# Kernel tuning notes

Hardware: AMD Instinct MI355X
Metric: run time of the kernel (lower is better)

The kernel has to match this reference:

```python
import jax, jax.numpy as jnp
import numpy as np

B, DIN, D = 1000, 1024, 512
C, L = 1203, 77
N_INS, N_EX = 4, 5
K_SEL, K_TOP = 32, 5
HEADS, DH, MLP, NL = 8, 64, 2048, 4
TEMP = 50.0


def setup_inputs() -> dict:
    key = jax.random.key(0)
    ks = iter(jax.random.split(key, 64))

    def rn(shape, s=0.02):
        return jax.random.normal(next(ks), shape, dtype=jnp.float32) * s

    def layer_params(prefix):
        return {
            prefix + '_ln1_g': jnp.ones((NL, D)), prefix + '_ln1_b': jnp.zeros((NL, D)),
            prefix + '_qkv_w': rn((NL, D, 3 * D)), prefix + '_qkv_b': jnp.zeros((NL, 3 * D)),
            prefix + '_out_w': rn((NL, D, D)), prefix + '_out_b': jnp.zeros((NL, D)),
            prefix + '_ln2_g': jnp.ones((NL, D)), prefix + '_ln2_b': jnp.zeros((NL, D)),
            prefix + '_fc_w': rn((NL, D, MLP)), prefix + '_fc_b': jnp.zeros((NL, MLP)),
            prefix + '_pr_w': rn((NL, MLP, D)), prefix + '_pr_b': jnp.zeros((NL, D)),
        }

    zw = jax.random.normal(next(ks), (D, C + 1), dtype=jnp.float32)
    zw = zw / jnp.linalg.norm(zw, axis=0, keepdims=True)  # F.normalize(dim=0) as in __init__
    inp = {
        'x': jax.random.normal(next(ks), (B, DIN), dtype=jnp.float32),
        'linear_w': rn((DIN, D)), 'linear_b': jnp.zeros((D,)),
        'zs_weight': zw,
        'sample_w': rn((D, D)), 'sample_b': jnp.zeros((D,)),
        'ins_token': rn((N_INS, D), 0.1),
        'token_seq': rn((C, L, D), 0.1),
        'exemplar': rn((C, N_EX, D), 0.1),
        'eos_index': jax.random.randint(next(ks), (C,), 5, 60, dtype=jnp.int32),
    }
    inp.update(layer_params('agg'))
    inp['pos_emb'] = rn((L, D), 0.01)
    inp.update(layer_params('txt'))
    inp['lnf_g'] = jnp.ones((D,))
    inp['lnf_b'] = jnp.zeros((D,))
    inp['text_proj'] = rn((D, D))
    return inp


def layernorm(x, g, b, eps=1e-5):
    m = x.mean(-1, keepdims=True)
    v = x.var(-1, keepdims=True)
    return (x - m) * jax.lax.rsqrt(v + eps) * g + b


def quick_gelu(x):  # CLIP QuickGELU
    return x * jax.nn.sigmoid(1.702 * x)


def transformer(h, ln1g, ln1b, qkvw, qkvb, ow, ob, ln2g, ln2b, fcw, fcb, prw, prb, mask=None):
    # h: [N, S, D]; pre-LN residual attention blocks (CLIP style)
    Bn, S, _ = h.shape
    scale = np.float32(1.0 / np.sqrt(DH))
    for i in range(NL):
        a = layernorm(h, ln1g[i], ln1b[i])
        qkv = a @ qkvw[i] + qkvb[i]
        q, k, v = jnp.split(qkv, 3, axis=-1)
        q = q.reshape(Bn, S, HEADS, DH)
        k = k.reshape(Bn, S, HEADS, DH)
        v = v.reshape(Bn, S, HEADS, DH)
        s = jnp.einsum('bqhd,bkhd->bhqk', q, k) * scale
        if mask is not None:
            s = s + mask
        o = jnp.einsum('bhqk,bkhd->bqhd', jax.nn.softmax(s, axis=-1), v).reshape(Bn, S, D)
        h = h + o @ ow[i] + ob[i]
        m = layernorm(h, ln2g[i], ln2b[i])
        h = h + quick_gelu(m @ fcw[i] + fcb[i]) @ prw[i] + prb[i]
    return h


def inverse_sigmoid(x, eps=1e-5):
    x = jnp.clip(x, 0.0, 1.0)
    x1 = jnp.clip(x, eps, None)
    x2 = jnp.clip(1.0 - x, eps, None)
    return jnp.log(x1 / x2)


def reference(x, linear_w, linear_b, zs_weight, sample_w, sample_b, ins_token, token_seq,
              exemplar, eos_index,
              agg_ln1_g, agg_ln1_b, agg_qkv_w, agg_qkv_b, agg_out_w, agg_out_b,
              agg_ln2_g, agg_ln2_b, agg_fc_w, agg_fc_b, agg_pr_w, agg_pr_b,
              pos_emb, txt_ln1_g, txt_ln1_b, txt_qkv_w, txt_qkv_b, txt_out_w, txt_out_b,
              txt_ln2_g, txt_ln2_b, txt_fc_w, txt_fc_b, txt_pr_w, txt_pr_b,
              lnf_g, lnf_b, text_proj):
    # ---- base classifier ----
    h = x @ linear_w + linear_b                                        # [B, D]
    h = TEMP * h / jnp.linalg.norm(h, axis=1, keepdims=True)
    logits = h @ zs_weight                                             # [B, C+1]
    # ---- entropy-based proposal selection (eval path, k=32) ----
    p = jax.nn.sigmoid(logits)
    entropy = (-p * jax.nn.log_sigmoid(logits)).sum(-1)                # [B]
    _, select_index = jax.lax.top_k(entropy, K_SEL)                    # [32]
    sel_logits = logits[select_index]                                  # [32, C+1]
    _, topk_index = jax.lax.top_k(sel_logits[:, :-1], K_TOP)           # [32, 5]
    sampled_x = jax.lax.stop_gradient(h[select_index]) @ sample_w + sample_b  # [32, D]
    # ---- batched aggregator input (replaces per-proposal python loop) ----
    base = ins_token[None] + (sampled_x / TEMP)[:, None, :]            # [32, N_INS, D]
    base = jnp.broadcast_to(base[:, None], (K_SEL, K_TOP, N_INS, D))
    ex = exemplar[topk_index]                                          # [32, 5, N_EX, D]
    agg_in = jnp.concatenate([base, ex], axis=2).reshape(K_SEL * K_TOP, N_INS + N_EX, D)
    agg_out = transformer(agg_in, agg_ln1_g, agg_ln1_b, agg_qkv_w, agg_qkv_b, agg_out_w,
                          agg_out_b, agg_ln2_g, agg_ln2_b, agg_fc_w, agg_fc_b, agg_pr_w, agg_pr_b)
    ins_tokens = agg_out[:, :N_INS].reshape(K_SEL, K_TOP, N_INS, D)
    # ---- splice instance tokens into class prompts ----
    prompt = token_seq[topk_index]                                     # [32, 5, L, D]
    upd = jnp.concatenate([prompt[:, :, :2], ins_tokens, prompt[:, :, 2:L - N_INS]], axis=2)
    # ---- CLIP text encoder on updated prompts ----
    t = upd.reshape(K_SEL * K_TOP, L, D) + pos_emb
    causal = jnp.where(jnp.tril(jnp.ones((L, L), bool)), 0.0, -1e9).astype(jnp.float32)
    t = transformer(t, txt_ln1_g, txt_ln1_b, txt_qkv_w, txt_qkv_b, txt_out_w, txt_out_b,
                    txt_ln2_g, txt_ln2_b, txt_fc_w, txt_fc_b, txt_pr_w, txt_pr_b, mask=causal)
    t = layernorm(t, lnf_g, lnf_b)
    eos = (eos_index[topk_index] + 2 * N_INS).reshape(-1)              # [160]
    feats = t[jnp.arange(K_SEL * K_TOP), eos] @ text_proj              # [160, D]
    feats = feats / jnp.linalg.norm(feats, axis=-1, keepdims=True)
    rerank_logits = jnp.einsum('sd,skd->sk', sampled_x, feats.reshape(K_SEL, K_TOP, D))
    # ---- fuse + scatter back ----
    sel_det = jax.lax.stop_gradient(sel_logits)
    sel_topk = jnp.take_along_axis(sel_det, topk_index, axis=1)
    fused = jax.nn.sigmoid(sel_topk) ** 0.75 * jax.nn.sigmoid(rerank_logits) ** 0.25
    reranked = inverse_sigmoid(fused)
    rows = jnp.arange(K_SEL)[:, None]
    logits_clone = sel_det.at[rows, topk_index].set(reranked)
    logits_final = logits.at[select_index].set(logits_clone)
    return logits, rerank_logits, select_index, logits_final
```

## Files before the change

kernel.cpp:

```cpp
#include <hip/hip_runtime.h>
#include <math.h>

#define TID ((int)threadIdx.x)

constexpr int Bsz = 1000, DIN = 1024, Dm = 512, C1 = 1204, C0 = 1203, Ltok = 77;
constexpr int NINS = 4, NEX = 5, KSEL = 32, KTOP = 5, NHEAD = 8, DH = 64, MLPD = 2048, NL = 4, Pn = 160;
constexpr float TEMPc = 50.0f;

typedef __attribute__((ext_vector_type(8))) short short8;
typedef __attribute__((ext_vector_type(4))) float f32x4;
typedef __attribute__((address_space(1))) const void g1void;
typedef __attribute__((address_space(3))) void l3void;
#define GLOAD16(g, l) __builtin_amdgcn_global_load_lds((g1void*)(g), (l3void*)(l), 16, 0, 0)

__device__ __forceinline__ float sigf(float z) {
  return z >= 0.f ? 1.f / (1.f + expf(-z)) : expf(z) / (1.f + expf(z));
}

__device__ __forceinline__ float qgelu(float v) {
  return v * __fdividef(1.f, 1.f + __expf(-1.702f * v));
}

__device__ __forceinline__ unsigned short f2bfu(float f) {
  unsigned u = __builtin_bit_cast(unsigned, f);
  u += 0x7fffu + ((u >> 16) & 1u);
  return (unsigned short)(u >> 16);
}
__device__ __forceinline__ short f2bf(float f) { return (short)f2bfu(f); }

__global__ __launch_bounds__(256, 4) void bgemm_k(const short* __restrict__ A,
                                                  const short* __restrict__ Bt,
                                                  const float* __restrict__ bias,
                                                  float* __restrict__ Cf,
                                                  short* __restrict__ Cb,
                                                  float* __restrict__ Xres,
                                                  int M, int N, int K, int mode) {
  __shared__ short As[8192];
  __shared__ short Bs[8192];
  int nwg = gridDim.x * gridDim.y;
  int orig = blockIdx.y * gridDim.x + blockIdx.x;
  int xcd = orig & 7, lid = orig >> 3;
  int q = nwg >> 3, r = nwg & 7;
  int swz = (xcd < r ? xcd * (q + 1) : r * (q + 1) + (xcd - r) * q) + lid;
  int row0 = (swz / gridDim.x) * 128, col0 = (swz % gridDim.x) * 128;
  int lane = TID & 63;
  int w = TID >> 6;
  int wr = (TID >> 7) & 1, wc = (TID >> 6) & 1;
  int skb = (TID >> 4) & 3, si = TID & 15;
  f32x4 acc[4][4] = {};
  int nt = K >> 6;
  int kb = lane >> 4, i = lane & 15;
  for (int t = 0; t < nt; ++t) {
#pragma unroll
    for (int s = 0; s < 2; ++s) {
#pragma unroll
      for (int c = 0; c < 2; ++c) {
        int row = (c * 4 + w) * 16 + si;
        int k0 = (t << 6) + (s << 5) + skb * 8;
        GLOAD16(A + (size_t)(row0 + row) * K + k0, As + s * 4096 + (c * 256 + w * 64) * 8);
        GLOAD16(Bt + (size_t)(col0 + row) * K + k0, Bs + s * 4096 + (c * 256 + w * 64) * 8);
      }
    }
    __syncthreads();
#pragma unroll
    for (int s = 0; s < 2; ++s) {
      const short* Ab = As + s * 4096;
      const short* Bb = Bs + s * 4096;
      short8 af[4], bfr[4];
#pragma unroll
      for (int m = 0; m < 4; ++m)
        af[m] = *(const short8*)(Ab + ((((wr * 4 + m) * 4 + kb) * 16 + i) * 8));
#pragma unroll
      for (int n = 0; n < 4; ++n)
        bfr[n] = *(const short8*)(Bb + ((((wc * 4 + n) * 4 + kb) * 16 + i) * 8));
#pragma unroll
      for (int m = 0; m < 4; ++m)
#pragma unroll
        for (int n = 0; n < 4; ++n)
          acc[m][n] = __builtin_amdgcn_mfma_f32_16x16x32_bf16(bfr[n], af[m], acc[m][n], 0, 0, 0);
    }
    __syncthreads();
  }
  int li = lane & 15, lg = lane >> 4;
#pragma unroll
  for (int m = 0; m < 4; ++m) {
    int row = row0 + wr * 64 + m * 16 + li;
    if (row >= M) continue;
#pragma unroll
    for (int n = 0; n < 4; ++n) {
      int colb = col0 + wc * 64 + n * 16 + lg * 4;
      f32x4 v = acc[m][n];
      if (bias) {
        float4 bv = *(const float4*)(bias + colb);
        v[0] += bv.x; v[1] += bv.y; v[2] += bv.z; v[3] += bv.w;
      }
      size_t off = (size_t)row * N + colb;
      if (mode == 0) {
        *(float4*)(Cf + off) = make_float4(v[0], v[1], v[2], v[3]);
      } else if (mode == 1) {
        float4* p = (float4*)(Xres + off);
        float4 o = *p;
        o.x += v[0]; o.y += v[1]; o.z += v[2]; o.w += v[3];
        *p = o;
      } else {
        if (mode == 2) {
          v[0] = qgelu(v[0]); v[1] = qgelu(v[1]); v[2] = qgelu(v[2]); v[3] = qgelu(v[3]);
        }
        uint2 pk;
        pk.x = (unsigned)f2bfu(v[0]) | ((unsigned)f2bfu(v[1]) << 16);
        pk.y = (unsigned)f2bfu(v[2]) | ((unsigned)f2bfu(v[3]) << 16);
        *(uint2*)(Cb + off) = pk;
      }
    }
  }
}

__global__ __launch_bounds__(256) void wconv_k(const float* __restrict__ W,
                                               short* __restrict__ Wt, int K, int N) {
  int l = blockIdx.z;
  const float* Wl = W + (size_t)l * K * N;
  short* Wtl = Wt + (size_t)l * K * N;
  __shared__ float t[32][33];
  int n0 = blockIdx.x * 32, k0 = blockIdx.y * 32;
  int tx = TID & 31, ty = TID >> 5;
#pragma unroll
  for (int u = 0; u < 4; ++u)
    t[ty + u * 8][tx] = Wl[(size_t)(k0 + ty + u * 8) * N + n0 + tx];
  __syncthreads();
#pragma unroll
  for (int u = 0; u < 4; ++u)
    Wtl[(size_t)(n0 + ty + u * 8) * K + k0 + tx] = f2bf(t[tx][ty + u * 8]);
}

__global__ __launch_bounds__(256) void gemm32s_k(const float* __restrict__ A,
                                                 const float* __restrict__ W,
                                                 float* __restrict__ P,
                                                 int M, int N, int K, int KC) {
  __shared__ float As[64][17];
  __shared__ float Ws[16][65];
  int tx = TID & 15, ty = TID >> 4;
  int row0 = blockIdx.y * 64, col0 = blockIdx.x * 64;
  int kbeg = blockIdx.z * KC;
  int kend = kbeg + KC < K ? kbeg + KC : K;
  float acc[4][4] = {};
  for (int k0 = kbeg; k0 < kend; k0 += 16) {
    {
      int r = TID >> 2, c4 = (TID & 3) * 4;
      int gr = row0 + r;
#pragma unroll
      for (int u = 0; u < 4; ++u) {
        int gc = k0 + c4 + u;
        As[r][c4 + u] = (gr < M && gc < K) ? A[gr * K + gc] : 0.f;
      }
    }
    {
      int c = TID & 63;
      int gc = col0 + c;
#pragma unroll
      for (int u = 0; u < 4; ++u) {
        int rr = (TID >> 6) * 4 + u;
        int gk = k0 + rr;
        Ws[rr][c] = (gk < K && gc < N) ? W[gk * N + gc] : 0.f;
      }
    }
    __syncthreads();
#pragma unroll
    for (int kk = 0; kk < 16; ++kk) {
      float a[4], b[4];
#pragma unroll
      for (int i = 0; i < 4; ++i) a[i] = As[ty * 4 + i][kk];
#pragma unroll
      for (int j = 0; j < 4; ++j) b[j] = Ws[kk][tx * 4 + j];
#pragma unroll
      for (int i = 0; i < 4; ++i)
#pragma unroll
        for (int j = 0; j < 4; ++j) acc[i][j] += a[i] * b[j];
    }
    __syncthreads();
  }
  float* Ps = P + (size_t)blockIdx.z * M * N;
#pragma unroll
  for (int i = 0; i < 4; ++i) {
    int rrow = row0 + ty * 4 + i;
    if (rrow >= M) continue;
#pragma unroll
    for (int j = 0; j < 4; ++j) {
      int ccol = col0 + tx * 4 + j;
      if (ccol >= N) continue;
      Ps[(size_t)rrow * N + ccol] = acc[i][j];
    }
  }
}

__global__ __launch_bounds__(256) void reduce_k(const float* __restrict__ P,
                                                const float* __restrict__ bias,
                                                float* __restrict__ C,
                                                float* __restrict__ C2,
                                                int MN, int N, int S) {
  int i = blockIdx.x * 256 + TID;
  if (i >= MN) return;
  float v = 0.f;
  for (int s = 0; s < S; ++s) v += P[(size_t)s * MN + i];
  if (bias) v += bias[i % N];
  C[i] = v;
  if (C2) C2[i] = v;
}

__global__ __launch_bounds__(256) void rownorm_k(float* __restrict__ h) {
  int r = blockIdx.x;
  float* x = h + r * Dm;
  float v0 = x[TID], v1 = x[TID + 256];
  __shared__ float s1[256];
  s1[TID] = v0 * v0 + v1 * v1;
  __syncthreads();
  for (int s = 128; s; s >>= 1) { if (TID < s) s1[TID] += s1[TID + s]; __syncthreads(); }
  float sc = TEMPc / sqrtf(s1[0]);
  x[TID] = v0 * sc;
  x[TID + 256] = v1 * sc;
}

__global__ __launch_bounds__(256) void entropy_k(const float* __restrict__ logits,
                                                 double* __restrict__ ent) {
  int r = blockIdx.x;
  double acc = 0.0;
  for (int c = TID; c < C1; c += 256) {
    float z = logits[r * C1 + c];
    float ls = z >= 0.f ? -log1pf(expf(-z)) : z - log1pf(expf(z));
    float p = z >= 0.f ? 1.f / (1.f + expf(-z)) : expf(z) / (1.f + expf(z));
    acc += (double)(-p * ls);
  }
  __shared__ double sd[256];
  sd[TID] = acc;
  __syncthreads();
  for (int s = 128; s; s >>= 1) { if (TID < s) sd[TID] += sd[TID + s]; __syncthreads(); }
  if (TID == 0) ent[r] = sd[0];
}

__global__ __launch_bounds__(256) void top32_k(const double* __restrict__ ent,
                                               int* __restrict__ selidx,
                                               float* __restrict__ out2) {
  __shared__ double v[1000];
  __shared__ double wv[4];
  __shared__ int wi[4];
  for (int i = TID; i < 1000; i += 256) v[i] = ent[i];
  __syncthreads();
  int w = TID >> 6, lane = TID & 63;
  for (int r = 0; r < KSEL; ++r) {
    double bv = -1e300; int bi = 1 << 30;
    for (int i = TID; i < 1000; i += 256) {
      double x = v[i];
      if (x > bv || (x == bv && i < bi)) { bv = x; bi = i; }
    }
#pragma unroll
    for (int off = 32; off; off >>= 1) {
      double ov = __shfl_xor(bv, off, 64);
      int oi = __shfl_xor(bi, off, 64);
      if (ov > bv || (ov == bv && oi < bi)) { bv = ov; bi = oi; }
    }
    if (lane == 0) { wv[w] = bv; wi[w] = bi; }
    __syncthreads();
    if (TID == 0) {
      double fv = wv[0]; int fi = wi[0];
#pragma unroll
      for (int u = 1; u < 4; ++u)
        if (wv[u] > fv || (wv[u] == fv && wi[u] < fi)) { fv = wv[u]; fi = wi[u]; }
      selidx[r] = fi; out2[r] = (float)fi; v[fi] = -1e300;
    }
    __syncthreads();
  }
}

__global__ __launch_bounds__(256) void top5_k(const float* __restrict__ logits,
                                              const int* __restrict__ selidx,
                                              int* __restrict__ topk) {
  int s = blockIdx.x;
  int row = selidx[s];
  __shared__ float v[C0];
  __shared__ float wv[4];
  __shared__ int wi[4];
  for (int i = TID; i < C0; i += 256) v[i] = logits[row * C1 + i];
  __syncthreads();
  int w = TID >> 6, lane = TID & 63;
  for (int r = 0; r < KTOP; ++r) {
    float bv = -INFINITY; int bi = 1 << 30;
    for (int i = TID; i < C0; i += 256) {
      float x = v[i];
      if (x > bv || (x == bv && i < bi)) { bv = x; bi = i; }
    }
#pragma unroll
    for (int off = 32; off; off >>= 1) {
      float ov = __shfl_xor(bv, off, 64);
      int oi = __shfl_xor(bi, off, 64);
      if (ov > bv || (ov == bv && oi < bi)) { bv = ov; bi = oi; }
    }
    if (lane == 0) { wv[w] = bv; wi[w] = bi; }
    __syncthreads();
    if (TID == 0) {
      float fv = wv[0]; int fi = wi[0];
#pragma unroll
      for (int u = 1; u < 4; ++u)
        if (wv[u] > fv || (wv[u] == fv && wi[u] < fi)) { fv = wv[u]; fi = wi[u]; }
      topk[s * KTOP + r] = fi; v[fi] = -INFINITY;
    }
    __syncthreads();
  }
}

__global__ void eos_k(const int* __restrict__ eos_index, const int* __restrict__ topk,
                      int* __restrict__ eosl) {
  for (int p = TID; p < Pn; p += 256) eosl[p] = eos_index[topk[p]] + 2 * NINS;
}

__global__ void gather_h_k(const float* __restrict__ h, const int* __restrict__ selidx,
                           float* __restrict__ hsel) {
  int s = blockIdx.x;
  int row = selidx[s];
  for (int d = TID; d < Dm; d += 256) hsel[s * Dm + d] = h[row * Dm + d];
}

__global__ __launch_bounds__(256) void build_agg_k(const float* __restrict__ ins,
                                                   const float* __restrict__ sampled,
                                                   const float* __restrict__ ex,
                                                   const int* __restrict__ topk,
                                                   float* __restrict__ X) {
  int b = blockIdx.x;
  int p = b / 9, tok = b % 9;
  int s = p / KTOP;
#pragma unroll
  for (int u = 0; u < 2; ++u) {
    int d = TID + u * 256;
    float v;
    if (tok < NINS) v = ins[tok * Dm + d] + sampled[s * Dm + d] * (1.f / TEMPc);
    else {
      int cls = topk[p];
      v = ex[(cls * NEX + (tok - NINS)) * Dm + d];
    }
    X[b * Dm + d] = v;
  }
}

__global__ void save_ins_k(const float* __restrict__ X, float* __restrict__ insbuf) {
  int p = blockIdx.x;
  for (int i = TID; i < NINS * Dm; i += 256) insbuf[p * NINS * Dm + i] = X[p * 9 * Dm + i];
}

__global__ __launch_bounds__(256) void build_txt_k(const float* __restrict__ token_seq,
                                                   const float* __restrict__ insbuf,
                                                   const float* __restrict__ pos,
                                                   const int* __restrict__ topk,
                                                   float* __restrict__ X, int p0) {
  int b = blockIdx.x;
  int pl = b / Ltok, tok = b % Ltok;
  int p = p0 + pl;
  int cls = topk[p];
#pragma unroll
  for (int u = 0; u < 2; ++u) {
    int d = TID + u * 256;
    float v;
    if (tok < 2) v = token_seq[(cls * Ltok + tok) * Dm + d];
    else if (tok < 2 + NINS) v = insbuf[(p * NINS + (tok - 2)) * Dm + d];
    else v = token_seq[(cls * Ltok + (tok - NINS)) * Dm + d];
    X[b * Dm + d] = v + pos[tok * Dm + d];
  }
}

__global__ __launch_bounds__(256) void ln_k(const float* __restrict__ X,
                                            const float* __restrict__ g,
                                            const float* __restrict__ b,
                                            short* __restrict__ A) {
  int t = blockIdx.x;
  const float* x = X + t * Dm;
  float v0 = x[TID], v1 = x[TID + 256];
  __shared__ float s1[256], s2[256];
  s1[TID] = v0 + v1;
  s2[TID] = v0 * v0 + v1 * v1;
  __syncthreads();
  for (int s = 128; s; s >>= 1) {
    if (TID < s) { s1[TID] += s1[TID + s]; s2[TID] += s2[TID + s]; }
    __syncthreads();
  }
  float mean = s1[0] * (1.f / 512.f);
  float var = s2[0] * (1.f / 512.f) - mean * mean;
  float inv = rsqrtf(var + 1e-5f);
  A[t * Dm + TID] = f2bf((v0 - mean) * inv * g[TID] + b[TID]);
  A[t * Dm + TID + 256] = f2bf((v1 - mean) * inv * g[TID + 256] + b[TID + 256]);
}

__global__ __launch_bounds__(320) void attn_tx_k(const short* __restrict__ qkv,
                                                 short* __restrict__ O, int S) {
  __shared__ short Kf[5120];
  __shared__ short Vt[6144];
  __shared__ short Pf[5][1536];
  int p = blockIdx.x >> 3, h = blockIdx.x & 7;
  int base = p * S;
  for (int c = TID; c < 640; c += 320) {
    int i = c & 15, kb = (c >> 4) & 7, g = c >> 7;
    int j = g * 16 + i;
    short8 v = {};
    if (j < S) v = *(const short8*)(qkv + (size_t)(base + j) * 1536 + 512 + h * 64 + kb * 8);
    *(short8*)(Kf + c * 8) = v;
  }
  for (int c = TID; c < 640; c += 320) {
    int j = c >> 3;
    int d0 = (c & 7) * 8;
    short8 v = {};
    if (j < S) v = *(const short8*)(qkv + (size_t)(base + j) * 1536 + 1024 + h * 64 + d0);
    int kb = j >> 3, jj = j & 7;
#pragma unroll
    for (int u = 0; u < 8; ++u) {
      int d = d0 + u;
      Vt[(((d >> 4) * 12 + kb) * 16 + (d & 15)) * 8 + jj] = v[u];
    }
  }
  for (int c = TID; c < 128; c += 320) {
    int i = c & 15, kb = 10 + ((c >> 4) & 1), g = c >> 5;
    *(short8*)(Vt + ((g * 12 + kb) * 16 + i) * 8) = short8{};
  }
  __syncthreads();
  int w = TID >> 6, lane = TID & 63;
  int li = lane & 15, lg = lane >> 4;
  short8 aq[2];
#pragma unroll
  for (int ks = 0; ks < 2; ++ks)
    aq[ks] = *(const short8*)(qkv + (size_t)(base + w * 16 + li) * 1536 + h * 64 + ks * 32 + lg * 8);
  f32x4 accs[5] = {};
#pragma unroll
  for (int t = 0; t < 5; ++t)
#pragma unroll
    for (int ks = 0; ks < 2; ++ks) {
      short8 bk = *(const short8*)(Kf + ((t * 8 + ks * 4 + lg) * 16 + li) * 8);
      accs[t] = __builtin_amdgcn_mfma_f32_16x16x32_bf16(aq[ks], bk, accs[t], 0, 0, 0);
    }
  int rowg = w * 16 + lg * 4;
#pragma unroll
  for (int r = 0; r < 4; ++r) {
    int row = rowg + r;
    float v[5];
    float mx = -1e30f;
#pragma unroll
    for (int t = 0; t < 5; ++t) {
      int col = t * 16 + li;
      float x = accs[t][r] * 0.125f;
      bool ok = (col < S) && (col <= row);
      v[t] = ok ? x : -1e30f;
      mx = fmaxf(mx, v[t]);
    }
#pragma unroll
    for (int off = 1; off < 16; off <<= 1) mx = fmaxf(mx, __shfl_xor(mx, off, 64));
    float sum = 0.f;
#pragma unroll
    for (int t = 0; t < 5; ++t) {
      v[t] = (v[t] > -1e29f) ? __expf(v[t] - mx) : 0.f;
      sum += v[t];
    }
#pragma unroll
    for (int off = 1; off < 16; off <<= 1) sum += __shfl_xor(sum, off, 64);
    float inv = __fdividef(1.f, sum);
#pragma unroll
    for (int t = 0; t < 5; ++t) {
      int c = t * 16 + li;
      Pf[w][((c >> 3) * 16 + (row - w * 16)) * 8 + (c & 7)] = f2bf(v[t] * inv);
    }
  }
  for (int z = lane; z < 256; z += 64) {
    int kb = 10 + (z >> 7);
    int rem = z & 127;
    Pf[w][(kb * 16 + (rem >> 3)) * 8 + (rem & 7)] = 0;
  }
  f32x4 acco[4] = {};
#pragma unroll
  for (int s = 0; s < 3; ++s) {
    short8 ap = *(const short8*)(Pf[w] + ((s * 4 + lg) * 16 + li) * 8);
#pragma unroll
    for (int n = 0; n < 4; ++n) {
      short8 bv = *(const short8*)(Vt + ((n * 12 + s * 4 + lg) * 16 + li) * 8);
      acco[n] = __builtin_amdgcn_mfma_f32_16x16x32_bf16(ap, bv, acco[n], 0, 0, 0);
    }
  }
#pragma unroll
  for (int n = 0; n < 4; ++n)
#pragma unroll
    for (int r = 0; r < 4; ++r) {
      int row = rowg + r;
      if (row < S) O[(size_t)(base + row) * 512 + h * 64 + n * 16 + li] = f2bf(acco[n][r]);
    }
}

__global__ __launch_bounds__(256) void attn_k(const float* __restrict__ qkv,
                                              short* __restrict__ O, int S, int causal) {
  int blk = blockIdx.x;
  int p = blk >> 3, h = blk & 7;
  __shared__ float Qs[Ltok][68], Ks[Ltok][68], Vs[Ltok][68];
  __shared__ float ps[4][132];
  int base = p * S;
  for (int idx = TID; idx < S * 16; idx += 256) {
    int j = idx >> 4, c = idx & 15;
    const float4* q = (const float4*)(qkv + (size_t)(base + j) * 1536 + h * 64);
    const float4* k = (const float4*)(qkv + (size_t)(base + j) * 1536 + 512 + h * 64);
    const float4* v = (const float4*)(qkv + (size_t)(base + j) * 1536 + 1024 + h * 64);
    ((float4*)&Qs[j][0])[c] = q[c];
    ((float4*)&Ks[j][0])[c] = k[c];
    ((float4*)&Vs[j][0])[c] = v[c];
  }
  __syncthreads();
  int wave = TID >> 6, lane = TID & 63;
  bool val0 = lane < S, val1 = lane + 64 < S;
  int j0 = val0 ? lane : 0;
  int j1 = val1 ? lane + 64 : 0;
  const float4* k0p = (const float4*)&Ks[j0][0];
  const float4* k1p = (const float4*)&Ks[j1][0];
  for (int i = wave; i < S; i += 4) {
    const float4* q4 = (const float4*)&Qs[i][0];
    float a0 = 0.f, a1 = 0.f;
#pragma unroll
    for (int d4 = 0; d4 < 16; ++d4) {
      float4 qv = q4[d4], k0v = k0p[d4], k1v = k1p[d4];
      a0 += qv.x * k0v.x + qv.y * k0v.y + qv.z * k0v.z + qv.w * k0v.w;
      a1 += qv.x * k1v.x + qv.y * k1v.y + qv.z * k1v.z + qv.w * k1v.w;
    }
    float m0 = (val0 && (!causal || lane <= i)) ? a0 * 0.125f : -1e30f;
    float m1 = (val1 && (!causal || lane + 64 <= i)) ? a1 * 0.125f : -1e30f;
    float mx = fmaxf(m0, m1);
#pragma unroll
    for (int off = 32; off; off >>= 1) mx = fmaxf(mx, __shfl_xor(mx, off, 64));
    float e0 = expf(m0 - mx), e1 = expf(m1 - mx);
    float sum = e0 + e1;
#pragma unroll
    for (int off = 32; off; off >>= 1) sum += __shfl_xor(sum, off, 64);
    float inv = 1.f / sum;
    ps[wave][lane] = e0 * inv;
    ps[wave][lane + 64] = e1 * inv;
    float o = 0.f;
    for (int j = 0; j < S; ++j) o += ps[wave][j] * Vs[j][lane];
    O[(base + i) * Dm + h * 64 + lane] = f2bf(o);
  }
}

__global__ __launch_bounds__(256) void feats_k(const float* __restrict__ X,
                                               const int* __restrict__ eosl,
                                               const float* __restrict__ g,
                                               const float* __restrict__ bb,
                                               const float* __restrict__ proj,
                                               float* __restrict__ feats, int p0) {
  int pl = blockIdx.x;
  int p = p0 + pl;
  int e = eosl[p];
  const float* x = X + (size_t)(pl * Ltok + e) * Dm;
  __shared__ float row[Dm];
  __shared__ float s1[256], s2[256];
  float v0 = x[TID], v1 = x[TID + 256];
  s1[TID] = v0 + v1;
  s2[TID] = v0 * v0 + v1 * v1;
  __syncthreads();
  for (int s = 128; s; s >>= 1) {
    if (TID < s) { s1[TID] += s1[TID + s]; s2[TID] += s2[TID + s]; }
    __syncthreads();
  }
  float mean = s1[0] * (1.f / 512.f);
  float var = s2[0] * (1.f / 512.f) - mean * mean;
  float inv = rsqrtf(var + 1e-5f);
  row[TID] = (v0 - mean) * inv * g[TID] + bb[TID];
  row[TID + 256] = (v1 - mean) * inv * g[TID + 256] + bb[TID + 256];
  __syncthreads();
  float a0 = 0.f, a1 = 0.f;
  for (int d = 0; d < Dm; ++d) {
    float r = row[d];
    a0 += r * proj[d * Dm + TID];
    a1 += r * proj[d * Dm + TID + 256];
  }
  s1[TID] = a0 * a0 + a1 * a1;
  __syncthreads();
  for (int s = 128; s; s >>= 1) { if (TID < s) s1[TID] += s1[TID + s]; __syncthreads(); }
  float sc = 1.f / sqrtf(s1[0]);
  feats[p * Dm + TID] = a0 * sc;
  feats[p * Dm + TID + 256] = a1 * sc;
}

__global__ void rerank_k(const float* __restrict__ sampled, const float* __restrict__ feats,
                         const int* __restrict__ selidx, const int* __restrict__ topk,
                         const float* __restrict__ logits, float* __restrict__ out1,
                         float* __restrict__ out3) {
  int idx = blockIdx.x;
  int s = idx / KTOP;
  int lane = TID;
  float acc = 0.f;
  for (int d = lane; d < Dm; d += 64) acc += sampled[s * Dm + d] * feats[idx * Dm + d];
#pragma unroll
  for (int off = 32; off; off >>= 1) acc += __shfl_down(acc, off, 64);
  if (lane == 0) {
    out1[idx] = acc;
    int row = selidx[s];
    int cls = topk[idx];
    float sl = logits[row * C1 + cls];
    float a = sigf(sl), b = sigf(acc);
    float fused = powf(a, 0.75f) * powf(b, 0.25f);
    float xx = fminf(fmaxf(fused, 0.f), 1.f);
    float x1 = fmaxf(xx, 1e-5f);
    float x2 = fmaxf(1.f - xx, 1e-5f);
    out3[row * C1 + cls] = logf(x1 / x2);
  }
}

static inline size_t alup(size_t x) { return (x + 255) & ~(size_t)255; }

constexpr size_t WT_QKV = (size_t)NL * Dm * 3 * Dm;
constexpr size_t WT_OUT = (size_t)NL * Dm * Dm;
constexpr size_t WT_FC  = (size_t)NL * Dm * MLPD;
constexpr size_t WT_PR  = (size_t)NL * MLPD * Dm;
constexpr size_t WT_ALL = WT_QKV + WT_OUT + WT_FC + WT_PR;

static void plan_rows(int PC, size_t* rows_o, size_t* RP_o) {
  size_t rows = (size_t)PC * Ltok;
  if (rows < (size_t)(Pn * 9)) rows = Pn * 9;
  size_t RP = (rows + 127) & ~(size_t)127;
  *rows_o = rows; *RP_o = RP;
}

static size_t plan_bytes(int PC) {
  size_t rows, RP;
  plan_rows(PC, &rows, &RP);
  size_t tot = 0;
  tot += alup(Bsz * Dm * 4);
  tot += alup(Bsz * 8);
  tot += alup(KSEL * 4);
  tot += alup(Pn * 4);
  tot += alup(Pn * 4);
  tot += alup(KSEL * Dm * 4);
  tot += alup(KSEL * Dm * 4);
  tot += alup(Pn * NINS * Dm * 4);
  tot += alup(Pn * Dm * 4);
  tot += alup(rows * Dm * 4);
  tot += alup(RP * Dm * 2);
  tot += alup(RP * Dm * 2);
  tot += alup((size_t)(Pn * 9) * 3 * Dm * 4);
  tot += alup(RP * 3 * Dm * 2);
  tot += alup(RP * MLPD * 2);
  tot += 2 * alup(WT_ALL * 2);
  tot += alup((size_t)8 * Bsz * Dm * 4);
  tot += alup((size_t)4 * Bsz * C1 * 4);
  tot += alup((size_t)8 * KSEL * Dm * 4);
  return tot;
}

extern "C" void kernel_launch(void* const* d_in, const int* in_sizes, int n_in,
                              void* d_out, int out_size, void* d_ws, size_t ws_size,
                              hipStream_t stream) {
  const float* x         = (const float*)d_in[0];
  const float* linear_w  = (const float*)d_in[1];
  const float* linear_b  = (const float*)d_in[2];
  const float* zs_w      = (const float*)d_in[3];
  const float* sample_w  = (const float*)d_in[4];
  const float* sample_b  = (const float*)d_in[5];
  const float* ins_token = (const float*)d_in[6];
  const float* token_seq = (const float*)d_in[7];
  const float* exemplar  = (const float*)d_in[8];
  const int*   eos_index = (const int*)d_in[9];
  const float* agg_ln1_g = (const float*)d_in[10];
  const float* agg_ln1_b = (const float*)d_in[11];
  const float* agg_qkv_w = (const float*)d_in[12];
  const float* agg_qkv_b = (const float*)d_in[13];
  const float* agg_out_w = (const float*)d_in[14];
  const float* agg_out_b = (const float*)d_in[15];
  const float* agg_ln2_g = (const float*)d_in[16];
  const float* agg_ln2_b = (const float*)d_in[17];
  const float* agg_fc_w  = (const float*)d_in[18];
  const float* agg_fc_b  = (const float*)d_in[19];
  const float* agg_pr_w  = (const float*)d_in[20];
  const float* agg_pr_b  = (const float*)d_in[21];
  const float* pos_emb   = (const float*)d_in[22];
  const float* txt_ln1_g = (const float*)d_in[23];
  const float* txt_ln1_b = (const float*)d_in[24];
  const float* txt_qkv_w = (const float*)d_in[25];
  const float* txt_qkv_b = (const float*)d_in[26];
  const float* txt_out_w = (const float*)d_in[27];
  const float* txt_out_b = (const float*)d_in[28];
  const float* txt_ln2_g = (const float*)d_in[29];
  const float* txt_ln2_b = (const float*)d_in[30];
  const float* txt_fc_w  = (const float*)d_in[31];
  const float* txt_fc_b  = (const float*)d_in[32];
  const float* txt_pr_w  = (const float*)d_in[33];
  const float* txt_pr_b  = (const float*)d_in[34];
  const float* lnf_g     = (const float*)d_in[35];
  const float* lnf_b     = (const float*)d_in[36];
  const float* text_proj = (const float*)d_in[37];

  float* out0 = (float*)d_out;
  float* out1 = out0 + Bsz * C1;
  float* out2 = out1 + KSEL * KTOP;
  float* out3 = out2 + KSEL;

  int PC = 20;
  const int cands[4] = {160, 80, 40, 20};
  for (int i = 0; i < 4; ++i)
    if (plan_bytes(cands[i]) <= ws_size) { PC = cands[i]; break; }
  int NC = Pn / PC;

  char* wp = (char*)d_ws;
  auto carve = [&](size_t bytes) -> void* { void* r = (void*)wp; wp += alup(bytes); return r; };
  size_t rows, RP;
  plan_rows(PC, &rows, &RP);

  float* h       = (float*)carve(Bsz * Dm * 4);
  double* ent    = (double*)carve(Bsz * 8);
  int* selidx    = (int*)carve(KSEL * 4);
  int* topk      = (int*)carve(Pn * 4);
  int* eosl      = (int*)carve(Pn * 4);
  float* hsel    = (float*)carve(KSEL * Dm * 4);
  float* sampled = (float*)carve(KSEL * Dm * 4);
  float* insbuf  = (float*)carve(Pn * NINS * Dm * 4);
  float* feats   = (float*)carve(Pn * Dm * 4);
  float* X       = (float*)carve(rows * Dm * 4);
  short* Abuf    = (short*)carve(RP * Dm * 2);
  short* Obuf    = (short*)carve(RP * Dm * 2);
  float* QKV     = (float*)carve((size_t)(Pn * 9) * 3 * Dm * 4);
  short* QKVb    = (short*)carve(RP * 3 * Dm * 2);
  short* Hb      = (short*)carve(RP * MLPD * 2);
  short* wtA     = (short*)carve(WT_ALL * 2);
  short* wtT     = (short*)carve(WT_ALL * 2);
  float* Plin    = (float*)carve((size_t)8 * Bsz * Dm * 4);
  float* Pzs     = (float*)carve((size_t)4 * Bsz * C1 * 4);
  float* Psmp    = (float*)carve((size_t)8 * KSEL * Dm * 4);

  short* wtA_qkv = wtA;
  short* wtA_out = wtA_qkv + WT_QKV;
  short* wtA_fc  = wtA_out + WT_OUT;
  short* wtA_pr  = wtA_fc + WT_FC;
  short* wtT_qkv = wtT;
  short* wtT_out = wtT_qkv + WT_QKV;
  short* wtT_fc  = wtT_out + WT_OUT;
  short* wtT_pr  = wtT_fc + WT_FC;

  dim3 blk(256);
  auto wconv = [&](const float* W, short* Wt, int K, int N) {
    dim3 g(N / 32, K / 32, NL);
    wconv_k<<<g, blk, 0, stream>>>(W, Wt, K, N);
  };
  auto bgemm = [&](const short* A, const short* Wt, const float* bias, float* Cf, short* Cb,
                   float* Xres, int M, int N, int K, int mode) {
    dim3 g(N / 128, (M + 127) / 128);
    bgemm_k<<<g, blk, 0, stream>>>(A, Wt, bias, Cf, Cb, Xres, M, N, K, mode);
  };
  auto gemm32s = [&](const float* A, const float* W, float* P, int M, int N, int K, int S) {
    dim3 g((N + 63) / 64, (M + 63) / 64, S);
    gemm32s_k<<<g, blk, 0, stream>>>(A, W, P, M, N, K, K / S);
  };
  auto reduce = [&](const float* P, const float* bias, float* C, float* C2, int MN, int N, int S) {
    reduce_k<<<(MN + 255) / 256, blk, 0, stream>>>(P, bias, C, C2, MN, N, S);
  };

  wconv(agg_qkv_w, wtA_qkv, Dm, 3 * Dm);
  wconv(agg_out_w, wtA_out, Dm, Dm);
  wconv(agg_fc_w,  wtA_fc,  Dm, MLPD);
  wconv(agg_pr_w,  wtA_pr,  MLPD, Dm);
  wconv(txt_qkv_w, wtT_qkv, Dm, 3 * Dm);
  wconv(txt_out_w, wtT_out, Dm, Dm);
  wconv(txt_fc_w,  wtT_fc,  Dm, MLPD);
  wconv(txt_pr_w,  wtT_pr,  MLPD, Dm);

  gemm32s(x, linear_w, Plin, Bsz, Dm, DIN, 8);
  reduce(Plin, linear_b, h, nullptr, Bsz * Dm, Dm, 8);
  rownorm_k<<<Bsz, blk, 0, stream>>>(h);
  gemm32s(h, zs_w, Pzs, Bsz, C1, Dm, 4);
  reduce(Pzs, nullptr, out0, out3, Bsz * C1, C1, 4);
  entropy_k<<<Bsz, blk, 0, stream>>>(out0, ent);
  top32_k<<<1, blk, 0, stream>>>(ent, selidx, out2);
  top5_k<<<KSEL, blk, 0, stream>>>(out0, selidx, topk);
  eos_k<<<1, blk, 0, stream>>>(eos_index, topk, eosl);
  gather_h_k<<<KSEL, blk, 0, stream>>>(h, selidx, hsel);
  gemm32s(hsel, sample_w, Psmp, KSEL, Dm, Dm, 8);
  reduce(Psmp, sample_b, sampled, nullptr, KSEL * Dm, Dm, 8);

  build_agg_k<<<Pn * 9, blk, 0, stream>>>(ins_token, sampled, exemplar, topk, X);
  {
    int M = Pn * 9;
    for (int i = 0; i < NL; ++i) {
      ln_k<<<M, blk, 0, stream>>>(X, agg_ln1_g + i * Dm, agg_ln1_b + i * Dm, Abuf);
      bgemm(Abuf, wtA_qkv + (size_t)i * Dm * 3 * Dm, agg_qkv_b + i * 3 * Dm, QKV, nullptr, nullptr, M, 3 * Dm, Dm, 0);
      attn_k<<<Pn * NHEAD, blk, 0, stream>>>(QKV, Obuf, 9, 0);
      bgemm(Obuf, wtA_out + (size_t)i * Dm * Dm, agg_out_b + i * Dm, nullptr, nullptr, X, M, Dm, Dm, 1);
      ln_k<<<M, blk, 0, stream>>>(X, agg_ln2_g + i * Dm, agg_ln2_b + i * Dm, Abuf);
      bgemm(Abuf, wtA_fc + (size_t)i * Dm * MLPD, agg_fc_b + i * MLPD, nullptr, Hb, nullptr, M, MLPD, Dm, 2);
      bgemm(Hb, wtA_pr + (size_t)i * MLPD * Dm, agg_pr_b + i * Dm, nullptr, nullptr, X, M, Dm, MLPD, 1);
    }
  }
  save_ins_k<<<Pn, blk, 0, stream>>>(X, insbuf);

  for (int c = 0; c < NC; ++c) {
    int p0 = c * PC;
    int M = PC * Ltok;
    build_txt_k<<<PC * Ltok, blk, 0, stream>>>(token_seq, insbuf, pos_emb, topk, X, p0);
    for (int i = 0; i < NL; ++i) {
      ln_k<<<M, blk, 0, stream>>>(X, txt_ln1_g + i * Dm, txt_ln1_b + i * Dm, Abuf);
      bgemm(Abuf, wtT_qkv + (size_t)i * Dm * 3 * Dm, txt_qkv_b + i * 3 * Dm, nullptr, QKVb, nullptr, M, 3 * Dm, Dm, 3);
      attn_tx_k<<<dim3(PC * NHEAD), dim3(320), 0, stream>>>(QKVb, Obuf, Ltok);
      bgemm(Obuf, wtT_out + (size_t)i * Dm * Dm, txt_out_b + i * Dm, nullptr, nullptr, X, M, Dm, Dm, 1);
      ln_k<<<M, blk, 0, stream>>>(X, txt_ln2_g + i * Dm, txt_ln2_b + i * Dm, Abuf);
      bgemm(Abuf, wtT_fc + (size_t)i * Dm * MLPD, txt_fc_b + i * MLPD, nullptr, Hb, nullptr, M, MLPD, Dm, 2);
      bgemm(Hb, wtT_pr + (size_t)i * MLPD * Dm, txt_pr_b + i * Dm, nullptr, nullptr, X, M, Dm, MLPD, 1);
    }
    feats_k<<<PC, blk, 0, stream>>>(X, eosl, lnf_g, lnf_b, text_proj, feats, p0);
  }

  rerank_k<<<Pn, dim3(64), 0, stream>>>(sampled, feats, selidx, topk, out0, out1, out3);
}
```

Before: 1.975 ms.

## Split-K the narrow residual GEMMs with a separate bias-plus-residual reduce

Adds a split-K bf16 MFMA GEMM kernel that writes fp32 partial tiles to a workspace, plus a reduction kernel that sums the partials, adds the bias and accumulates into the residual stream. It replaces the out-projection (split 2) and MLP down-projection (split 4) GEMMs in both transformers, which have N=512 and so launch few workgroups. The aim is more parallelism on these underfilled launches. The cost is extra partial-sum traffic through global memory and one additional kernel launch per GEMM.

```diff
diff --git a/kernel.cpp b/kernel.cpp
--- a/kernel.cpp
+++ b/kernel.cpp
@@ -115,6 +115,82 @@
   }
 }
 
+__global__ __launch_bounds__(256, 4) void bgemm_sk_k(const short* __restrict__ A,
+                                                     const short* __restrict__ Bt,
+                                                     float* __restrict__ P,
+                                                     int M, int N, int K, int KC) {
+  __shared__ short As[8192];
+  __shared__ short Bs[8192];
+  int nwg = gridDim.x * gridDim.y;
+  int orig = blockIdx.y * gridDim.x + blockIdx.x;
+  int xcd = orig & 7, lid = orig >> 3;
+  int q = nwg >> 3, r = nwg & 7;
+  int swz = (xcd < r ? xcd * (q + 1) : r * (q + 1) + (xcd - r) * q) + lid;
+  int row0 = (swz / gridDim.x) * 128, col0 = (swz % gridDim.x) * 128;
+  int kbeg = blockIdx.z * KC;
+  int lane = TID & 63;
+  int w = TID >> 6;
+  int wr = (TID >> 7) & 1, wc = (TID >> 6) & 1;
+  int skb = (TID >> 4) & 3, si = TID & 15;
+  f32x4 acc[4][4] = {};
+  int nt = KC >> 6;
+  int kb = lane >> 4, i = lane & 15;
+  for (int t = 0; t < nt; ++t) {
+#pragma unroll
+    for (int s = 0; s < 2; ++s) {
+#pragma unroll
+      for (int c = 0; c < 2; ++c) {
+        int row = (c * 4 + w) * 16 + si;
+        int k0 = kbeg + (t << 6) + (s << 5) + skb * 8;
+        GLOAD16(A + (size_t)(row0 + row) * K + k0, As + s * 4096 + (c * 256 + w * 64) * 8);
+        GLOAD16(Bt + (size_t)(col0 + row) * K + k0, Bs + s * 4096 + (c * 256 + w * 64) * 8);
+      }
+    }
+    __syncthreads();
+#pragma unroll
+    for (int s = 0; s < 2; ++s) {
+      const short* Ab = As + s * 4096;
+      const short* Bb = Bs + s * 4096;
+      short8 af[4], bfr[4];
+#pragma unroll
+      for (int m = 0; m < 4; ++m)
+        af[m] = *(const short8*)(Ab + ((((wr * 4 + m) * 4 + kb) * 16 + i) * 8));
+#pragma unroll
+      for (int n = 0; n < 4; ++n)
+        bfr[n] = *(const short8*)(Bb + ((((wc * 4 + n) * 4 + kb) * 16 + i) * 8));
+#pragma unroll
+      for (int m = 0; m < 4; ++m)
+#pragma unroll
+        for (int n = 0; n < 4; ++n)
+          acc[m][n] = __builtin_amdgcn_mfma_f32_16x16x32_bf16(bfr[n], af[m], acc[m][n], 0, 0, 0);
+    }
+    __syncthreads();
+  }
+  float* Pz = P + (size_t)blockIdx.z * M * N;
+  int li = lane & 15, lg = lane >> 4;
+#pragma unroll
+  for (int m = 0; m < 4; ++m) {
+    int row = row0 + wr * 64 + m * 16 + li;
+    if (row >= M) continue;
+#pragma unroll
+    for (int n = 0; n < 4; ++n) {
+      int colb = col0 + wc * 64 + n * 16 + lg * 4;
+      *(float4*)(Pz + (size_t)row * N + colb) = make_float4(acc[m][n][0], acc[m][n][1], acc[m][n][2], acc[m][n][3]);
+    }
+  }
+}
+
+__global__ __launch_bounds__(256) void reduce_res_k(const float* __restrict__ P,
+                                                    const float* __restrict__ bias,
+                                                    float* __restrict__ Xres,
+                                                    int MN, int N, int S) {
+  int i = blockIdx.x * 256 + TID;
+  if (i >= MN) return;
+  float v = bias[i % N];
+  for (int s = 0; s < S; ++s) v += P[(size_t)s * MN + i];
+  Xres[i] += v;
+}
+
 __global__ __launch_bounds__(256) void wconv_k(const float* __restrict__ W,
                                                short* __restrict__ Wt, int K, int N) {
   int l = blockIdx.z;
@@ -639,6 +715,7 @@
   tot += alup((size_t)8 * Bsz * Dm * 4);
   tot += alup((size_t)4 * Bsz * C1 * 4);
   tot += alup((size_t)8 * KSEL * Dm * 4);
+  tot += alup((size_t)4 * RP * Dm * 4);
   return tot;
 }
 
@@ -720,6 +797,7 @@
   float* Plin    = (float*)carve((size_t)8 * Bsz * Dm * 4);
   float* Pzs     = (float*)carve((size_t)4 * Bsz * C1 * 4);
   float* Psmp    = (float*)carve((size_t)8 * KSEL * Dm * 4);
+  float* Psk     = (float*)carve((size_t)4 * RP * Dm * 4);
 
   short* wtA_qkv = wtA;
   short* wtA_out = wtA_qkv + WT_QKV;
@@ -739,6 +817,13 @@
                    float* Xres, int M, int N, int K, int mode) {
     dim3 g(N / 128, (M + 127) / 128);
     bgemm_k<<<g, blk, 0, stream>>>(A, Wt, bias, Cf, Cb, Xres, M, N, K, mode);
+  };
+  auto bgemm_res_sk = [&](const short* A, const short* Wt, const float* bias, float* Xres,
+                          int M, int N, int K, int S) {
+    dim3 g(N / 128, (M + 127) / 128, S);
+    bgemm_sk_k<<<g, blk, 0, stream>>>(A, Wt, Psk, M, N, K, K / S);
+    int MN = M * N;
+    reduce_res_k<<<(MN + 255) / 256, blk, 0, stream>>>(Psk, bias, Xres, MN, N, S);
   };
   auto gemm32s = [&](const float* A, const float* W, float* P, int M, int N, int K, int S) {
     dim3 g((N + 63) / 64, (M + 63) / 64, S);
@@ -777,10 +862,10 @@
       ln_k<<<M, blk, 0, stream>>>(X, agg_ln1_g + i * Dm, agg_ln1_b + i * Dm, Abuf);
       bgemm(Abuf, wtA_qkv + (size_t)i * Dm * 3 * Dm, agg_qkv_b + i * 3 * Dm, QKV, nullptr, nullptr, M, 3 * Dm, Dm, 0);
       attn_k<<<Pn * NHEAD, blk, 0, stream>>>(QKV, Obuf, 9, 0);
-      bgemm(Obuf, wtA_out + (size_t)i * Dm * Dm, agg_out_b + i * Dm, nullptr, nullptr, X, M, Dm, Dm, 1);
+      bgemm_res_sk(Obuf, wtA_out + (size_t)i * Dm * Dm, agg_out_b + i * Dm, X, M, Dm, Dm, 2);
       ln_k<<<M, blk, 0, stream>>>(X, agg_ln2_g + i * Dm, agg_ln2_b + i * Dm, Abuf);
       bgemm(Abuf, wtA_fc + (size_t)i * Dm * MLPD, agg_fc_b + i * MLPD, nullptr, Hb, nullptr, M, MLPD, Dm, 2);
-      bgemm(Hb, wtA_pr + (size_t)i * MLPD * Dm, agg_pr_b + i * Dm, nullptr, nullptr, X, M, Dm, MLPD, 1);
+      bgemm_res_sk(Hb, wtA_pr + (size_t)i * MLPD * Dm, agg_pr_b + i * Dm, X, M, Dm, MLPD, 4);
     }
   }
   save_ins_k<<<Pn, blk, 0, stream>>>(X, insbuf);
@@ -793,10 +878,10 @@
       ln_k<<<M, blk, 0, stream>>>(X, txt_ln1_g + i * Dm, txt_ln1_b + i * Dm, Abuf);
       bgemm(Abuf, wtT_qkv + (size_t)i * Dm * 3 * Dm, txt_qkv_b + i * 3 * Dm, nullptr, QKVb, nullptr, M, 3 * Dm, Dm, 3);
       attn_tx_k<<<dim3(PC * NHEAD), dim3(320), 0, stream>>>(QKVb, Obuf, Ltok);
-      bgemm(Obuf, wtT_out + (size_t)i * Dm * Dm, txt_out_b + i * Dm, nullptr, nullptr, X, M, Dm, Dm, 1);
+      bgemm_res_sk(Obuf, wtT_out + (size_t)i * Dm * Dm, txt_out_b + i * Dm, X, M, Dm, Dm, 2);
       ln_k<<<M, blk, 0, stream>>>(X, txt_ln2_g + i * Dm, txt_ln2_b + i * Dm, Abuf);
       bgemm(Abuf, wtT_fc + (size_t)i * Dm * MLPD, txt_fc_b + i * MLPD, nullptr, Hb, nullptr, M, MLPD, Dm, 2);
-      bgemm(Hb, wtT_pr + (size_t)i * MLPD * Dm, txt_pr_b + i * Dm, nullptr, nullptr, X, M, Dm, MLPD, 1);
+      bgemm_res_sk(Hb, wtT_pr + (size_t)i * MLPD * Dm, txt_pr_b + i * Dm, X, M, Dm, MLPD, 4);
     }
     feats_k<<<PC, blk, 0, stream>>>(X, eosl, lnf_g, lnf_b, text_proj, feats, p0);
   }
```

Result: no change. 1.990 ms (+0.8%).
